# Kernel tuning notes

Measured on AMD Instinct MI355X. Metric: run time of the kernel, lower is better.

The kernel has to match this reference:

```python
import jax, jax.numpy as jnp
import numpy as np

N = 100000
E = 1600000
F_IN = 128
HDIM = 64
HEADS = 8
C1 = HDIM // HEADS  # 8 per-head channels in conv1
NUM_CLASSES = 2
NUM_GRAPHS = 64
NEG_SLOPE = 0.2


def setup_inputs() -> dict:
    key = jax.random.key(0)
    ks = jax.random.split(key, 12)
    x = jax.random.normal(ks[0], (N, F_IN), dtype=jnp.float32)
    edge_index = jax.random.randint(ks[1], (2, E), 0, N, dtype=jnp.int64)
    batch = jnp.sort(jax.random.randint(ks[2], (N,), 0, NUM_GRAPHS, dtype=jnp.int64))
    # conv1 params (Glorot-ish scale)
    W1 = jax.random.normal(ks[3], (F_IN, HEADS * C1), dtype=jnp.float32) * (1.0 / np.sqrt(F_IN))
    att_src1 = jax.random.normal(ks[4], (HEADS, C1), dtype=jnp.float32) * 0.1
    att_dst1 = jax.random.normal(ks[5], (HEADS, C1), dtype=jnp.float32) * 0.1
    b1 = jnp.zeros((HEADS * C1,), dtype=jnp.float32)
    # conv2 params (1 head, no concat)
    W2 = jax.random.normal(ks[6], (HDIM, 1 * NUM_CLASSES), dtype=jnp.float32) * (1.0 / np.sqrt(HDIM))
    att_src2 = jax.random.normal(ks[7], (1, NUM_CLASSES), dtype=jnp.float32) * 0.1
    att_dst2 = jax.random.normal(ks[8], (1, NUM_CLASSES), dtype=jnp.float32) * 0.1
    b2 = jnp.zeros((NUM_CLASSES,), dtype=jnp.float32)
    return {"x": x, "edge_index": edge_index, "batch": batch,
            "W1": W1, "att_src1": att_src1, "att_dst1": att_dst1, "b1": b1,
            "W2": W2, "att_src2": att_src2, "att_dst2": att_dst2, "b2": b2}


def gat_conv(x, src, dst, W, a_src, a_dst, b, heads, ch, concat):
    # PyG GATConv: linear proj -> per-edge attention -> segment softmax over dst -> scatter-add
    n = x.shape[0]
    h = (x @ W).reshape(n, heads, ch)                      # [N,H,C]
    alpha_s = jnp.einsum('nhc,hc->nh', h, a_src)           # [N,H]
    alpha_d = jnp.einsum('nhc,hc->nh', h, a_dst)           # [N,H]
    e = jax.nn.leaky_relu(alpha_s[src] + alpha_d[dst], NEG_SLOPE)  # [E,H]
    m = jax.ops.segment_max(e, dst, num_segments=n)        # stable softmax per dst
    e = jnp.exp(e - m[dst])
    denom = jax.ops.segment_sum(e, dst, num_segments=n) + 1e-16
    alpha = e / denom[dst]                                 # [E,H]
    msg = h[src] * alpha[:, :, None]                       # [E,H,C]
    out = jax.ops.segment_sum(msg, dst, num_segments=n)    # [N,H,C]
    if concat:
        out = out.reshape(n, heads * ch)
    else:
        out = out.mean(axis=1)
    return out + b


def reference(x, edge_index, batch, W1, att_src1, att_dst1, b1, W2, att_src2, att_dst2, b2):
    # PyG GATConv default add_self_loops=True
    loops = jnp.arange(N, dtype=edge_index.dtype)
    src = jnp.concatenate([edge_index[0], loops])
    dst = jnp.concatenate([edge_index[1], loops])
    h = gat_conv(x, src, dst, W1, att_src1, att_dst1, b1, HEADS, C1, concat=True)
    h = jax.nn.relu(h)
    # F.dropout with training=False (eval mode) -> identity
    h = gat_conv(h, src, dst, W2, att_src2, att_dst2, b2, 1, NUM_CLASSES, concat=False)
    # global_mean_pool over batch ids
    sums = jax.ops.segment_sum(h, batch, num_segments=NUM_GRAPHS)
    cnts = jax.ops.segment_sum(jnp.ones((N,), h.dtype), batch, num_segments=NUM_GRAPHS)
    pooled = sums / jnp.maximum(cnts, 1.0)[:, None]        # [G, num_classes]
    return jax.nn.log_softmax(pooled, axis=1)
```

## Files before the change

kernel.cpp:

```cpp
#include <hip/hip_runtime.h>
#include <hip/hip_bf16.h>
#include <hip/hip_fp16.h>
#include <math.h>

#define NN 100000
#define EE 1600000
#define ET 1700000
#define NEG_SLOPE 0.2f
#define XS_STRIDE 136

#define BKB 8
#define BKSZ 256
#define NBUCK 391
#define SLAB 8192
#define PAD 32
#define EPT2 16
#define CHUNK2 (256 * EPT2)
#define NCH2 ((ET + CHUNK2 - 1) / CHUNK2)

typedef _Float16 f16;
typedef f16 f16x8 __attribute__((ext_vector_type(8)));
typedef float f32x4 __attribute__((ext_vector_type(4)));

__device__ __forceinline__ float leaky(float v) {
    return v > 0.f ? v : NEG_SLOPE * v;
}
__device__ __forceinline__ unsigned char enc_fp8(float v) {
    int pk = __builtin_amdgcn_cvt_pk_fp8_f32(v, 0.f, 0, false);
    return (unsigned char)(pk & 0xff);
}

__global__ __launch_bounds__(256) void convert_w_kernel(
        const float* __restrict__ W1, f16* __restrict__ wt) {
    int i = blockIdx.x * 256 + threadIdx.x;
    if (i < 128 * 64) {
        int n = i >> 7, k = i & 127;
        wt[n * 128 + k] = (f16)W1[k * 64 + n];
    }
}

__global__ __launch_bounds__(256) void gemm1_mfma(
        const float* __restrict__ x, const f16* __restrict__ wt,
        __half* __restrict__ h1, unsigned char* __restrict__ h1f8) {
    __shared__ f16 xs[64 * XS_STRIDE];
    const int tid = threadIdx.x;
    const int node0 = blockIdx.x * 64;
    for (int i = tid; i < 64 * 64; i += 256) {
        int r = i >> 6, cp = i & 63;
        int n = node0 + r;
        float2 v = (n < NN) ? ((const float2*)x)[(long)n * 64 + cp]
                            : make_float2(0.f, 0.f);
        xs[r * XS_STRIDE + 2 * cp]     = (f16)v.x;
        xs[r * XS_STRIDE + 2 * cp + 1] = (f16)v.y;
    }
    __syncthreads();
    const int wv = tid >> 6;
    const int lane = tid & 63;
    const int n16 = lane & 15;
    const int quad = lane >> 4;
    f16x8 bf[4][4];
#pragma unroll
    for (int t = 0; t < 4; ++t)
#pragma unroll
        for (int kk = 0; kk < 4; ++kk)
            bf[t][kk] = *(const f16x8*)(wt + ((t * 16 + n16) * 128 + kk * 32 + quad * 8));
    f32x4 acc[4] = {{0,0,0,0},{0,0,0,0},{0,0,0,0},{0,0,0,0}};
#pragma unroll
    for (int kk = 0; kk < 4; ++kk) {
        f16x8 af = *(const f16x8*)(xs + ((wv * 16 + n16) * XS_STRIDE + kk * 32 + quad * 8));
#pragma unroll
        for (int t = 0; t < 4; ++t)
            acc[t] = __builtin_amdgcn_mfma_f32_16x16x32_f16(af, bf[t][kk], acc[t], 0, 0, 0);
    }
#pragma unroll
    for (int t = 0; t < 4; ++t)
#pragma unroll
        for (int r = 0; r < 4; ++r) {
            int m = node0 + wv * 16 + quad * 4 + r;
            if (m < NN) {
                int idx = m * 64 + t * 16 + n16;
                h1[idx]   = __float2half_rn(acc[t][r]);
                h1f8[idx] = enc_fp8(acc[t][r]);
            }
        }
}

__global__ __launch_bounds__(256) void alpha1_kernel(
        const __half* __restrict__ h1, const float* __restrict__ att_s,
        const float* __restrict__ att_d,
        __half* __restrict__ as1h, float* __restrict__ alpha_d) {
    int i = blockIdx.x * 256 + threadIdx.x;
    if (i >= NN * 8) return;
    int h = i & 7;
    const __half* hp = h1 + (long)i * 8;
    float s = 0.f, d = 0.f;
#pragma unroll
    for (int c = 0; c < 8; ++c) {
        float v = __half2float(hp[c]);
        s += v * att_s[h * 8 + c];
        d += v * att_d[h * 8 + c];
    }
    as1h[i] = __float2half_rn(s);
    alpha_d[i] = d;
}

__global__ __launch_bounds__(256) void bucket_fill(
        const int* __restrict__ ei, int* __restrict__ bcur,
        unsigned* __restrict__ gpay) {
    __shared__ int lcnt[NBUCK];
    __shared__ int gbase[NBUCK];
    const int tid = threadIdx.x;
    for (int i = tid; i < NBUCK; i += 256) lcnt[i] = 0;
    __syncthreads();
    const int base = blockIdx.x * CHUNK2 + tid;
    unsigned pay[EPT2];
    int bk[EPT2], pos[EPT2];
#pragma unroll
    for (int k = 0; k < EPT2; ++k) {
        int e = base + k * 256;
        if (e < ET) {
            int s, d;
            if (e < EE) {
                s = __builtin_nontemporal_load(ei + e);
                d = __builtin_nontemporal_load(ei + EE + e);
            } else { s = d = e - EE; }
            int b = d >> BKB;
            bk[k] = b;
            pay[k] = ((unsigned)(d & (BKSZ - 1)) << 17) | (unsigned)s;
            pos[k] = atomicAdd(&lcnt[b], 1);
        } else bk[k] = -1;
    }
    __syncthreads();
    for (int i = tid; i < NBUCK; i += 256)
        gbase[i] = lcnt[i] ? (i * SLAB + atomicAdd(&bcur[i * PAD], lcnt[i])) : 0;
    __syncthreads();
#pragma unroll
    for (int k = 0; k < EPT2; ++k)
        if (bk[k] >= 0) gpay[gbase[bk[k]] + pos[k]] = pay[k];
}

__global__ __launch_bounds__(256) void fine_csr(
        const unsigned* __restrict__ gpay, const int* __restrict__ bcur,
        int* __restrict__ rowptr, int* __restrict__ rowend,
        int* __restrict__ csr_src) {
    __shared__ int cnt[BKSZ];
    __shared__ int ts[256];
    const int b = blockIdx.x;
    const int tid = threadIdx.x;
    const int off = b * SLAB;
    int blen = bcur[b * PAD];
    if (blen > SLAB) blen = SLAB;
    const int d0 = b << BKB;
    cnt[tid] = 0;
    __syncthreads();
    for (int i = tid; i < blen; i += 256)
        atomicAdd(&cnt[gpay[off + i] >> 17], 1);
    __syncthreads();
    int v = cnt[tid];
    ts[tid] = v;
    __syncthreads();
    for (int o = 1; o < 256; o <<= 1) {
        int u = (tid >= o) ? ts[tid - o] : 0;
        __syncthreads();
        ts[tid] += u;
        __syncthreads();
    }
    int excl = ts[tid] - v;
    cnt[tid] = excl;
    int d = d0 + tid;
    if (d < NN) {
        rowptr[d] = off + excl;
        rowend[d] = off + excl + v;
    }
    __syncthreads();
    for (int i = tid; i < blen; i += 256) {
        unsigned pay = gpay[off + i];
        int pos = atomicAdd(&cnt[pay >> 17], 1);
        csr_src[off + pos] = (int)(pay & 0x1FFFFu);
    }
}

__global__ __launch_bounds__(256) void conv1_fused_kernel(
        const int* __restrict__ rowptr, const int* __restrict__ rowend,
        const int* __restrict__ csr_src, const __half* __restrict__ as1h,
        const float* __restrict__ ad1,
        const unsigned char* __restrict__ h1f8, const float* __restrict__ b1,
        const float* __restrict__ W2, const float* __restrict__ as2,
        const float* __restrict__ ad2, float4* __restrict__ rec) {
    long gid = (long)blockIdx.x * 256 + threadIdx.x;
    int n = (int)(gid >> 6);
    if (n >= NN) return;
    n = __builtin_amdgcn_readfirstlane(n);
    int c = threadIdx.x & 63;
    int h = c >> 3;
    int kB = c >> 3;
    int hB = c & 7;
    float adh = ad1[n * 8 + h];
    float adB = ad1[n * 8 + hB];
    const int bperm_base = h << 2;
    int jb = rowptr[n], je = rowend[n];
    float l0 = 0.f, l1 = 0.f, l2 = 0.f, l3 = 0.f;
    float a0 = 0.f, a1 = 0.f, a2 = 0.f, a3 = 0.f;
    int j = jb;
    for (; j + 7 < je; j += 8) {
        int myS = csr_src[j + kB];
        float myp = __expf(leaky(__half2float(as1h[myS * 8 + hB]) + adB));
        int mypi = __float_as_int(myp);
#pragma unroll
        for (int k = 0; k < 8; ++k) {
            int sk = csr_src[j + k];
            float pk = __int_as_float(
                __builtin_amdgcn_ds_bpermute(bperm_base + (k << 5), mypi));
            float fk = __builtin_amdgcn_cvt_f32_fp8((int)h1f8[sk * 64 + c], 0);
            switch (k & 3) {
                case 0: l0 += pk; a0 += pk * fk; break;
                case 1: l1 += pk; a1 += pk * fk; break;
                case 2: l2 += pk; a2 += pk * fk; break;
                default: l3 += pk; a3 += pk * fk; break;
            }
        }
    }
    for (; j < je; ++j) {
        int s = csr_src[j];
        float p = __expf(leaky(__half2float(as1h[s * 8 + h]) + adh));
        float f = __builtin_amdgcn_cvt_f32_fp8((int)h1f8[s * 64 + c], 0);
        l0 += p;
        a0 += p * f;
    }
    float l = (l0 + l1) + (l2 + l3);
    float acc = (a0 + a1) + (a2 + a3);
    float o = acc / (l + 1e-16f);
    float a = o + b1[c];
    a = a > 0.f ? a : 0.f;
    float r0 = a * W2[c * 2];
    float r1 = a * W2[c * 2 + 1];
#pragma unroll
    for (int off = 32; off > 0; off >>= 1) {
        r0 += __shfl_xor(r0, off, 64);
        r1 += __shfl_xor(r1, off, 64);
    }
    if (c == 0) {
        float s2v = r0 * as2[0] + r1 * as2[1];
        float d2v = r0 * ad2[0] + r1 * ad2[1];
        rec[n] = make_float4(s2v, r0, r1, d2v);
    }
}

__global__ __launch_bounds__(256) void conv2_pool_kernel(
        const int* __restrict__ rowptr, const int* __restrict__ rowend,
        const int* __restrict__ csr_src, const float4* __restrict__ rec,
        const int* __restrict__ batch,
        float* __restrict__ pooled ) {
    __shared__ float ls[192];
    int tid = threadIdx.x;
    if (tid < 192) ls[tid] = 0.f;
    __syncthreads();
    int n = blockIdx.x * 256 + tid;
    if (n < NN) {
        float adn = rec[n].w;
        int jb = rowptr[n], je = rowend[n];
        float l0 = 0.f, l1 = 0.f, x0 = 0.f, x1 = 0.f, y0 = 0.f, y1 = 0.f;
        int j = jb;
        for (; j + 1 < je; j += 2) {
            float4 ra = rec[csr_src[j]];
            float4 rb = rec[csr_src[j + 1]];
            float pa = __expf(leaky(ra.x + adn));
            float pb = __expf(leaky(rb.x + adn));
            l0 += pa; x0 += pa * ra.y; y0 += pa * ra.z;
            l1 += pb; x1 += pb * rb.y; y1 += pb * rb.z;
        }
        for (; j < je; ++j) {
            float4 ra = rec[csr_src[j]];
            float pa = __expf(leaky(ra.x + adn));
            l0 += pa; x0 += pa * ra.y; y0 += pa * ra.z;
        }
        float inv = 1.f / (l0 + l1 + 1e-16f);
        int g = batch[n];
        atomicAdd(&ls[g * 2],     (x0 + x1) * inv);
        atomicAdd(&ls[g * 2 + 1], (y0 + y1) * inv);
        atomicAdd(&ls[128 + g],   1.f);
    }
    __syncthreads();
    if (tid < 192) atomicAdd(&pooled[tid], ls[tid]);
}

__global__ __launch_bounds__(64) void final_kernel(
        const float* __restrict__ pooled, const float* __restrict__ b2,
        float* __restrict__ out) {
    int g = threadIdx.x;
    if (g >= 64) return;
    float c = pooled[128 + g];
    float denom = c > 1.f ? c : 1.f;
    float p0 = pooled[g * 2] / denom + b2[0];
    float p1 = pooled[g * 2 + 1] / denom + b2[1];
    float m = fmaxf(p0, p1);
    float lse = m + logf(expf(p0 - m) + expf(p1 - m));
    out[g * 2] = p0 - lse;
    out[g * 2 + 1] = p1 - lse;
}

extern "C" void kernel_launch(void* const* d_in, const int* in_sizes, int n_in,
                              void* d_out, int out_size, void* d_ws, size_t ws_size,
                              hipStream_t stream) {
    const float* x   = (const float*)d_in[0];
    const int*   ei  = (const int*)d_in[1];
    const int*   bat = (const int*)d_in[2];
    const float* W1  = (const float*)d_in[3];
    const float* as1 = (const float*)d_in[4];
    const float* ad1 = (const float*)d_in[5];
    const float* b1  = (const float*)d_in[6];
    const float* W2  = (const float*)d_in[7];
    const float* as2 = (const float*)d_in[8];
    const float* ad2 = (const float*)d_in[9];
    const float* b2  = (const float*)d_in[10];
    float* out = (float*)d_out;

    float* ws = (float*)d_ws;
    const long off_h1     = 0;
    const long off_h1f8   = off_h1   + (long)NN * 32;
    const long off_wt     = off_h1f8 + (long)NN * 16;
    const long off_as1h   = off_wt   + 4096;
    const long off_ad1    = off_as1h + (long)NN * 4;
    const long off_rec    = off_ad1  + (long)NN * 8;
    const long off_rowptr = off_rec  + (long)NN * 4;
    const long off_rowend = off_rowptr + NN;
    const long off_gpay   = off_rowend + NN;
    const long off_csr    = off_gpay + (long)NBUCK * SLAB;
    const long off_zero   = off_csr  + (long)NBUCK * SLAB;
    const long off_bcur   = off_zero;
    const long off_pool   = off_bcur + NBUCK * PAD;
    const long zero_elems = off_pool + 192 - off_zero;

    hipMemsetAsync(ws + off_zero, 0, zero_elems * sizeof(float), stream);

    convert_w_kernel<<<32, 256, 0, stream>>>(W1, (f16*)(ws + off_wt));
    gemm1_mfma<<<(NN + 63) / 64, 256, 0, stream>>>(
        x, (const f16*)(ws + off_wt), (__half*)(ws + off_h1),
        (unsigned char*)(ws + off_h1f8));
    alpha1_kernel<<<(NN * 8 + 255) / 256, 256, 0, stream>>>(
        (const __half*)(ws + off_h1), as1, ad1,
        (__half*)(ws + off_as1h), ws + off_ad1);

    bucket_fill<<<NCH2, 256, 0, stream>>>(ei, (int*)(ws + off_bcur),
                                          (unsigned*)(ws + off_gpay));
    fine_csr<<<NBUCK, 256, 0, stream>>>(
        (const unsigned*)(ws + off_gpay), (const int*)(ws + off_bcur),
        (int*)(ws + off_rowptr), (int*)(ws + off_rowend),
        (int*)(ws + off_csr));

    conv1_fused_kernel<<<(int)(((long)NN * 64 + 255) / 256), 256, 0, stream>>>(
        (const int*)(ws + off_rowptr), (const int*)(ws + off_rowend),
        (const int*)(ws + off_csr), (const __half*)(ws + off_as1h),
        ws + off_ad1, (const unsigned char*)(ws + off_h1f8),
        b1, W2, as2, ad2, (float4*)(ws + off_rec));

    conv2_pool_kernel<<<(NN + 255) / 256, 256, 0, stream>>>(
        (const int*)(ws + off_rowptr), (const int*)(ws + off_rowend),
        (const int*)(ws + off_csr), (const float4*)(ws + off_rec),
        bat, ws + off_pool);

    final_kernel<<<1, 64, 0, stream>>>(ws + off_pool, b2, out);
}
```

Before: 258.2 us.

## Fuse attention-logit computation into GEMM epilogue and unroll conv2 gather by four

Attention source and destination logits are now computed inside the MFMA GEMM epilogue using cross-lane shuffles over each head's 8 channels. This removes the separate alpha1 kernel and the fp16 h1 buffer it read, saving a kernel launch and an N×64 half-precision write and re-read. The conv2 aggregation loop is also unrolled to four independent accumulators to expose more outstanding gathers. The logits now come from fp32 accumulators rather than fp16-rounded values, which slightly changes numerics.

```diff
diff --git a/kernel.cpp b/kernel.cpp
--- a/kernel.cpp
+++ b/kernel.cpp
@@ -41,7 +41,9 @@
 
 __global__ __launch_bounds__(256) void gemm1_mfma(
         const float* __restrict__ x, const f16* __restrict__ wt,
-        __half* __restrict__ h1, unsigned char* __restrict__ h1f8) {
+        const float* __restrict__ att_s, const float* __restrict__ att_d,
+        unsigned char* __restrict__ h1f8, __half* __restrict__ as1h,
+        float* __restrict__ ad1o) {
     __shared__ f16 xs[64 * XS_STRIDE];
     const int tid = threadIdx.x;
     const int node0 = blockIdx.x * 64;
@@ -72,36 +74,30 @@
         for (int t = 0; t < 4; ++t)
             acc[t] = __builtin_amdgcn_mfma_f32_16x16x32_f16(af, bf[t][kk], acc[t], 0, 0, 0);
     }
+    float ats[4], atd[4];
+#pragma unroll
+    for (int t = 0; t < 4; ++t) {
+        ats[t] = att_s[t * 16 + n16];
+        atd[t] = att_d[t * 16 + n16];
+    }
 #pragma unroll
     for (int t = 0; t < 4; ++t)
 #pragma unroll
         for (int r = 0; r < 4; ++r) {
             int m = node0 + wv * 16 + quad * 4 + r;
-            if (m < NN) {
-                int idx = m * 64 + t * 16 + n16;
-                h1[idx]   = __float2half_rn(acc[t][r]);
-                h1f8[idx] = enc_fp8(acc[t][r]);
+            bool ok = (m < NN);
+            if (ok) h1f8[m * 64 + t * 16 + n16] = enc_fp8(acc[t][r]);
+            float vs = acc[t][r] * ats[t];
+            float vd = acc[t][r] * atd[t];
+            vs += __shfl_xor(vs, 1, 64); vd += __shfl_xor(vd, 1, 64);
+            vs += __shfl_xor(vs, 2, 64); vd += __shfl_xor(vd, 2, 64);
+            vs += __shfl_xor(vs, 4, 64); vd += __shfl_xor(vd, 4, 64);
+            if (ok && (n16 & 7) == 0) {
+                int h = t * 2 + (n16 >> 3);
+                as1h[m * 8 + h] = __float2half_rn(vs);
+                ad1o[m * 8 + h] = vd;
             }
         }
-}
-
-__global__ __launch_bounds__(256) void alpha1_kernel(
-        const __half* __restrict__ h1, const float* __restrict__ att_s,
-        const float* __restrict__ att_d,
-        __half* __restrict__ as1h, float* __restrict__ alpha_d) {
-    int i = blockIdx.x * 256 + threadIdx.x;
-    if (i >= NN * 8) return;
-    int h = i & 7;
-    const __half* hp = h1 + (long)i * 8;
-    float s = 0.f, d = 0.f;
-#pragma unroll
-    for (int c = 0; c < 8; ++c) {
-        float v = __half2float(hp[c]);
-        s += v * att_s[h * 8 + c];
-        d += v * att_d[h * 8 + c];
-    }
-    as1h[i] = __float2half_rn(s);
-    alpha_d[i] = d;
 }
 
 __global__ __launch_bounds__(256) void bucket_fill(
@@ -259,25 +255,36 @@
     if (n < NN) {
         float adn = rec[n].w;
         int jb = rowptr[n], je = rowend[n];
-        float l0 = 0.f, l1 = 0.f, x0 = 0.f, x1 = 0.f, y0 = 0.f, y1 = 0.f;
+        float l0 = 0.f, l1 = 0.f, l2 = 0.f, l3 = 0.f;
+        float x0 = 0.f, x1 = 0.f, x2 = 0.f, x3 = 0.f;
+        float y0 = 0.f, y1 = 0.f, y2 = 0.f, y3 = 0.f;
         int j = jb;
-        for (; j + 1 < je; j += 2) {
+        for (; j + 3 < je; j += 4) {
             float4 ra = rec[csr_src[j]];
             float4 rb = rec[csr_src[j + 1]];
+            float4 rc = rec[csr_src[j + 2]];
+            float4 rd = rec[csr_src[j + 3]];
             float pa = __expf(leaky(ra.x + adn));
             float pb = __expf(leaky(rb.x + adn));
+            float pc = __expf(leaky(rc.x + adn));
+            float pd = __expf(leaky(rd.x + adn));
             l0 += pa; x0 += pa * ra.y; y0 += pa * ra.z;
             l1 += pb; x1 += pb * rb.y; y1 += pb * rb.z;
+            l2 += pc; x2 += pc * rc.y; y2 += pc * rc.z;
+            l3 += pd; x3 += pd * rd.y; y3 += pd * rd.z;
         }
         for (; j < je; ++j) {
             float4 ra = rec[csr_src[j]];
             float pa = __expf(leaky(ra.x + adn));
             l0 += pa; x0 += pa * ra.y; y0 += pa * ra.z;
         }
-        float inv = 1.f / (l0 + l1 + 1e-16f);
+        float l = (l0 + l1) + (l2 + l3);
+        float xx = (x0 + x1) + (x2 + x3);
+        float yy = (y0 + y1) + (y2 + y3);
+        float inv = 1.f / (l + 1e-16f);
         int g = batch[n];
-        atomicAdd(&ls[g * 2],     (x0 + x1) * inv);
-        atomicAdd(&ls[g * 2 + 1], (y0 + y1) * inv);
+        atomicAdd(&ls[g * 2],     xx * inv);
+        atomicAdd(&ls[g * 2 + 1], yy * inv);
         atomicAdd(&ls[128 + g],   1.f);
     }
     __syncthreads();
@@ -316,8 +323,7 @@
     float* out = (float*)d_out;
 
     float* ws = (float*)d_ws;
-    const long off_h1     = 0;
-    const long off_h1f8   = off_h1   + (long)NN * 32;
+    const long off_h1f8   = 0;
     const long off_wt     = off_h1f8 + (long)NN * 16;
     const long off_as1h   = off_wt   + 4096;
     const long off_ad1    = off_as1h + (long)NN * 4;
@@ -335,11 +341,9 @@
 
     convert_w_kernel<<<32, 256, 0, stream>>>(W1, (f16*)(ws + off_wt));
     gemm1_mfma<<<(NN + 63) / 64, 256, 0, stream>>>(
-        x, (const f16*)(ws + off_wt), (__half*)(ws + off_h1),
-        (unsigned char*)(ws + off_h1f8));
-    alpha1_kernel<<<(NN * 8 + 255) / 256, 256, 0, stream>>>(
-        (const __half*)(ws + off_h1), as1, ad1,
-        (__half*)(ws + off_as1h), ws + off_ad1);
+        x, (const f16*)(ws + off_wt), as1, ad1,
+        (unsigned char*)(ws + off_h1f8), (__half*)(ws + off_as1h),
+        ws + off_ad1);
 
     bucket_fill<<<NCH2, 256, 0, stream>>>(ei, (int*)(ws + off_bcur),
                                           (unsigned*)(ws + off_gpay));
```

Result: no change. 255.6 us (-1.0%).
